# Optimization experiments

Hardware: AMD Instinct MI355X
Metric: run time of the kernel (lower is better)

## Reference

```python
import jax, jax.numpy as jnp
import numpy as np

B, N, C = 2, 2048, 768
H = 12
HD = C // H
SCALE = HD ** -0.5


def setup_inputs() -> dict:
    key = jax.random.key(0)
    ks = jax.random.split(key, 5)
    s = 1.0 / np.sqrt(C)
    return {
        "x": jax.random.normal(ks[0], (B, N, C), dtype=jnp.float32),
        "Wq": jax.random.normal(ks[1], (C, C), dtype=jnp.float32) * s,
        "Wk": jax.random.normal(ks[2], (C, C), dtype=jnp.float32) * s,
        "Wv": jax.random.normal(ks[3], (C, C), dtype=jnp.float32) * s,
        "Wo": jax.random.normal(ks[4], (C, C), dtype=jnp.float32) * s,
        "bo": jnp.zeros((C,), dtype=jnp.float32),
    }


def reference(x, Wq, Wk, Wv, Wo, bo):
    b, n, c = x.shape
    # projections (equinox Linear: y = W @ x, i.e. x @ W.T); split heads -> [b, h, n, hd]
    q = (x @ Wq.T).reshape(b, n, H, HD).transpose(0, 2, 1, 3)
    k = (x @ Wk.T).reshape(b, n, H, HD).transpose(0, 2, 1, 3)
    v = (x @ Wv.T).reshape(b, n, H, HD).transpose(0, 2, 1, 3)
    # full O(N^2) score matrix, scaled dot-product
    scores = jnp.einsum("bhqd,bhkd->bhqk", q, k) * SCALE  # [b, h, n, n]
    probs = jax.nn.softmax(scores, axis=-1)
    # attn_drop = 0.0 -> identity
    out = jnp.einsum("bhqk,bhkd->bhqd", probs, v)  # [b, h, n, hd]
    out = out.transpose(0, 2, 1, 3).reshape(b, n, c)
    # output projection (proj_drop = 0.0 -> identity)
    return out @ Wo.T + bo
```

## Files before the change

kernel.cpp:

```cpp
#include <hip/hip_runtime.h>
#include <hip/hip_bf16.h>
#include <cstdint>

typedef __bf16 bf16;
typedef bf16 bf16x8 __attribute__((ext_vector_type(8)));
typedef float f32x4 __attribute__((ext_vector_type(4)));
typedef uint32_t u32;

#define MFMA16(a, b, c) __builtin_amdgcn_mfma_f32_16x16x32_bf16(a, b, c, 0, 0, 0)

static constexpr int Bb = 2, Hh = 12, Nn = 2048, Cc = 768, HD = 64;
static constexpr float SCALE_L2E = 0.125f * 1.4426950408889634f;

__device__ inline u32 pkbf(float a, float b) {
    union { struct { uint16_t lo, hi; } s; u32 w; } u;
    u.s.lo = __builtin_bit_cast(uint16_t, (bf16)a);
    u.s.hi = __builtin_bit_cast(uint16_t, (bf16)b);
    return u.w;
}

__device__ __forceinline__ size_t fidx(int bh, int n, int hd) {
    return ((size_t)(bh * 128 + (n >> 4)) * 2 + (hd >> 5)) * 512 +
           (size_t)(((hd >> 3) & 3) * 128 + (n & 15) * 8 + (hd & 7));
}
__device__ __forceinline__ size_t vidx(int bh, int n, int hd) {
    return (((size_t)(bh * 32 + (n >> 6)) * 4 + (hd >> 4)) * 2 + ((n >> 5) & 1)) * 512 +
           (size_t)(((n >> 3) & 3) * 128 + (hd & 15) * 8 + (n & 7));
}

__device__ __forceinline__ void stage16(const bf16* g, bf16* l) {
    __builtin_amdgcn_global_load_lds(
        (const __attribute__((address_space(1))) void*)g,
        (__attribute__((address_space(3))) void*)l, 16, 0, 0);
}

__device__ __forceinline__ void gload(bf16x8& d, const bf16* p) {
    asm volatile("global_load_dwordx4 %0, %1, off" : "=v"(d) : "v"(p));
}

#define VMWAIT(N) do { asm volatile("s_waitcnt vmcnt(" #N ")" ::); \
                       __builtin_amdgcn_sched_barrier(0); } while (0)

__global__ __launch_bounds__(256) void cvt_all(const float* __restrict__ x,
                                               const float* __restrict__ wq,
                                               const float* __restrict__ wk,
                                               const float* __restrict__ wv,
                                               const float* __restrict__ wo,
                                               bf16* __restrict__ xb,
                                               bf16* __restrict__ wqkv,
                                               bf16* __restrict__ wob) {
    const int b = blockIdx.x;
    const float* src;
    bf16* dst;
    int i;
    if (b < 1536) {
        src = x; dst = xb; i = b * 256 + threadIdx.x;
    } else {
        const int wbid  = b - 1536;
        const int which = wbid / 288;
        src = which == 0 ? wq : which == 1 ? wk : which == 2 ? wv : wo;
        dst = which == 3 ? wob : wqkv + (size_t)which * 589824;
        i = (wbid % 288) * 256 + threadIdx.x;
    }
    const float4* p = reinterpret_cast<const float4*>(src) + (size_t)i * 2;
    float4 v0 = p[0], v1 = p[1];
    bf16x8 o;
    o[0] = (bf16)v0.x; o[1] = (bf16)v0.y; o[2] = (bf16)v0.z; o[3] = (bf16)v0.w;
    o[4] = (bf16)v1.x; o[5] = (bf16)v1.y; o[6] = (bf16)v1.z; o[7] = (bf16)v1.w;
    reinterpret_cast<bf16x8*>(dst)[i] = o;
}

__global__ __launch_bounds__(256, 3) void gemm_qkv(const bf16* __restrict__ X,
                                                   const bf16* __restrict__ W,
                                                   bf16* __restrict__ QF,
                                                   bf16* __restrict__ KF,
                                                   bf16* __restrict__ VF) {
    const int m0      = blockIdx.x * 128;
    const int j00     = blockIdx.y * 128;
    const int grp     = blockIdx.y / 6;
    const int colbase = (blockIdx.y % 6) * 128;
    const int w   = threadIdx.x >> 6;
    const int wr  = w >> 1;
    const int wc  = w & 1;
    const int l   = threadIdx.x & 63;
    const int lr  = l & 15;
    const int lg  = l >> 4;

    __shared__ bf16 lsA[2][128 * 32];
    __shared__ bf16 lsB[2][128 * 32];

    const int lrow = l >> 2;
    const int lcol = (l & 3) * 8;

    auto STAGE = [&](int buf, int kk) {
#pragma unroll
        for (int i = 0; i < 2; i++) {
            const int s = w * 2 + i;
            stage16(X + (size_t)(m0 + s * 16 + lrow) * Cc + kk + lcol, &lsA[buf][s * 512]);
            stage16(W + (size_t)(j00 + s * 16 + lrow) * Cc + kk + lcol, &lsB[buf][s * 512]);
        }
    };

    f32x4 acc[4][4] = {};

    STAGE(0, 0);
    __syncthreads();
    int cur = 0;
#pragma unroll 1
    for (int it = 0; it < 24; ++it) {
        if (it < 23) STAGE(cur ^ 1, (it + 1) * 32);
        bf16x8 a[4], b[4];
#pragma unroll
        for (int r = 0; r < 4; r++)
            a[r] = *reinterpret_cast<const bf16x8*>(&lsA[cur][(wr * 64 + r * 16 + lr) * 32 + lg * 8]);
#pragma unroll
        for (int c = 0; c < 4; c++)
            b[c] = *reinterpret_cast<const bf16x8*>(&lsB[cur][(wc * 64 + c * 16 + lr) * 32 + lg * 8]);
        __builtin_amdgcn_s_setprio(1);
#pragma unroll
        for (int r = 0; r < 4; r++)
#pragma unroll
            for (int c = 0; c < 4; c++)
                acc[r][c] = MFMA16(a[r], b[c], acc[r][c]);
        __builtin_amdgcn_s_setprio(0);
        __syncthreads();
        cur ^= 1;
    }

#pragma unroll
    for (int r = 0; r < 4; r++)
#pragma unroll
        for (int c = 0; c < 4; c++)
#pragma unroll
            for (int j = 0; j < 4; j++) {
                const int m   = m0 + wr * 64 + r * 16 + lg * 4 + j;
                const int col = colbase + wc * 64 + c * 16 + lr;
                const int bb = m >> 11, n = m & 2047;
                const int h = col >> 6, hd = col & 63;
                const int bh = bb * Hh + h;
                const float v = acc[r][c][j];
                if (grp == 0) {
                    QF[fidx(bh, n, hd)] = (bf16)(v * SCALE_L2E);
                } else if (grp == 1) {
                    KF[fidx(bh, n, hd)] = (bf16)v;
                } else {
                    VF[vidx(bh, n, hd)] = (bf16)v;
                }
            }
}

__global__ __launch_bounds__(256) void gemm_proj(const bf16* __restrict__ X,
                                                 const bf16* __restrict__ W,
                                                 const float* __restrict__ bias,
                                                 float* __restrict__ Y) {
    const int m0 = blockIdx.x * 64;
    const int j0 = blockIdx.y * 64;
    const int w  = threadIdx.x >> 6;
    const int l  = threadIdx.x & 63;
    const int lr = l & 15;
    const int lg = l >> 4;

    __shared__ bf16 lsA[2][64 * 32];
    __shared__ bf16 lsB[2][64 * 32];

    const int lrow = l >> 2;
    const int lcol = (l & 3) * 8;

    auto STAGE = [&](int buf, int kk) {
        stage16(X + (size_t)(m0 + w * 16 + lrow) * Cc + kk + lcol, &lsA[buf][w * 512]);
        stage16(W + (size_t)(j0 + w * 16 + lrow) * Cc + kk + lcol, &lsB[buf][w * 512]);
    };

    f32x4 acc[4] = {};

    STAGE(0, 0);
    __syncthreads();
    int cur = 0;
#pragma unroll 1
    for (int it = 0; it < 24; ++it) {
        if (it < 23) STAGE(cur ^ 1, (it + 1) * 32);
        bf16x8 a = *reinterpret_cast<const bf16x8*>(&lsA[cur][(w * 16 + lr) * 32 + lg * 8]);
        bf16x8 b[4];
#pragma unroll
        for (int c = 0; c < 4; c++)
            b[c] = *reinterpret_cast<const bf16x8*>(&lsB[cur][(c * 16 + lr) * 32 + lg * 8]);
        __builtin_amdgcn_s_setprio(1);
#pragma unroll
        for (int c = 0; c < 4; c++)
            acc[c] = MFMA16(a, b[c], acc[c]);
        __builtin_amdgcn_s_setprio(0);
        __syncthreads();
        cur ^= 1;
    }

    const int mw = m0 + w * 16;
#pragma unroll
    for (int c = 0; c < 4; c++)
#pragma unroll
        for (int j = 0; j < 4; j++) {
            const int m   = mw + lg * 4 + j;
            const int col = j0 + c * 16 + lr;
            Y[(size_t)m * Cc + col] = acc[c][j] + bias[col];
        }
}

__global__ __launch_bounds__(256, 3) void attn_kernel(const bf16* __restrict__ QF,
                                                      const bf16* __restrict__ KF,
                                                      const bf16* __restrict__ VF,
                                                      bf16* __restrict__ AO) {
    const int bid  = (blockIdx.x & 7) * 96 + (blockIdx.x >> 3);
    const int qb   = bid & 31;
    const int bh   = bid >> 5;
    const int tid  = threadIdx.x;
    const int wid  = tid >> 6;
    const int team = wid >> 1;
    const int wt   = wid & 1;
    const int l    = tid & 63;
    const int lr   = l & 15;
    const int lg   = l >> 4;

    __shared__ bf16 vbuf[2][2][4096];
    __shared__ u32  p_lds[4][2][576];

    f32x4 acc[2][4] = {};
    f32x4 accs[2] = {};

    const bf16* Qbase = QF + ((size_t)(bh * 128 + qb * 4 + wt * 2) * 2) * 512 + l * 8;
    const bf16x8 qa0 = *reinterpret_cast<const bf16x8*>(Qbase);
    const bf16x8 qb0 = *reinterpret_cast<const bf16x8*>(Qbase + 512);
    const bf16x8 qa1 = *reinterpret_cast<const bf16x8*>(Qbase + 1024);
    const bf16x8 qb1 = *reinterpret_cast<const bf16x8*>(Qbase + 1536);

    bf16x8 ONES;
#pragma unroll
    for (int i = 0; i < 8; i++) ONES[i] = (bf16)1.0f;

    bf16x8 ka[8];
    const int tbase = team * 16;

    auto loadK = [&](int t) {
        const bf16* p = KF + ((size_t)bh * 256 + (tbase + t) * 8) * 512 + l * 8;
#pragma unroll
        for (int s = 0; s < 8; s++)
            gload(ka[s], p + (size_t)s * 512);
    };
    auto stageV = [&](int slot, int t) {
        const size_t tb = ((size_t)bh * 256 + (tbase + t) * 8) * 512;
#pragma unroll
        for (int i = 0; i < 4; i++) {
            const int s = wt * 4 + i;
            stage16(VF + tb + (size_t)s * 512 + l * 8, &vbuf[team][slot][s * 512]);
        }
    };

    const f32x4 fz = {0.f, 0.f, 0.f, 0.f};

    auto EXPPACK = [&](int f, const f32x4* s) {
#pragma unroll
        for (int st = 0; st < 4; st++) {
            float p0 = exp2f(s[st][0]);
            float p1 = exp2f(s[st][1]);
            float p2 = exp2f(s[st][2]);
            float p3 = exp2f(s[st][3]);
            *reinterpret_cast<uint2*>(&p_lds[wid][f][lr * 36 + st * 8 + lg * 2]) =
                make_uint2(pkbf(p0, p1), pkbf(p2, p3));
        }
    };

    stageV(0, 0);
    loadK(0);

#pragma unroll 1
    for (int t = 0; t < 16; ++t) {
        VMWAIT(0);
        __builtin_amdgcn_s_barrier();

        f32x4 s[4];
        __builtin_amdgcn_s_setprio(1);
#pragma unroll
        for (int st = 0; st < 4; st++) {
            s[st] = MFMA16(ka[st * 2], qa0, fz);
            s[st] = MFMA16(ka[st * 2 + 1], qb0, s[st]);
        }
        __builtin_amdgcn_s_setprio(0);
        EXPPACK(0, s);
        __builtin_amdgcn_s_setprio(1);
#pragma unroll
        for (int st = 0; st < 4; st++) {
            s[st] = MFMA16(ka[st * 2], qa1, fz);
            s[st] = MFMA16(ka[st * 2 + 1], qb1, s[st]);
        }
        __builtin_amdgcn_s_setprio(0);
        if (t < 15) {
            loadK(t + 1);
            stageV((t + 1) & 1, t + 1);
        }
        EXPPACK(1, s);

        asm volatile("s_waitcnt lgkmcnt(0)" ::: "memory");
        __builtin_amdgcn_sched_barrier(0);
        const bf16x8 pa00 = *reinterpret_cast<const bf16x8*>(&p_lds[wid][0][lr * 36 + lg * 4]);
        const bf16x8 pa01 = *reinterpret_cast<const bf16x8*>(&p_lds[wid][0][lr * 36 + 16 + lg * 4]);
        const bf16x8 pa10 = *reinterpret_cast<const bf16x8*>(&p_lds[wid][1][lr * 36 + lg * 4]);
        const bf16x8 pa11 = *reinterpret_cast<const bf16x8*>(&p_lds[wid][1][lr * 36 + 16 + lg * 4]);

        const bf16* vb = &vbuf[team][t & 1][l * 8];
        __builtin_amdgcn_s_setprio(1);
#pragma unroll
        for (int c = 0; c < 4; c++) {
            bf16x8 v0 = *reinterpret_cast<const bf16x8*>(vb + (c * 2) * 512);
            bf16x8 v1 = *reinterpret_cast<const bf16x8*>(vb + (c * 2 + 1) * 512);
            acc[0][c] = MFMA16(v0, pa00, acc[0][c]);
            acc[0][c] = MFMA16(v1, pa01, acc[0][c]);
            acc[1][c] = MFMA16(v0, pa10, acc[1][c]);
            acc[1][c] = MFMA16(v1, pa11, acc[1][c]);
        }
        accs[0] = MFMA16(ONES, pa00, accs[0]);
        accs[0] = MFMA16(ONES, pa01, accs[0]);
        accs[1] = MFMA16(ONES, pa10, accs[1]);
        accs[1] = MFMA16(ONES, pa11, accs[1]);
        __builtin_amdgcn_s_setprio(0);
    }

    __syncthreads();
    float* mrg = reinterpret_cast<float*>(&p_lds[0][0][0]);
    if (team == 1) {
#pragma unroll
        for (int f = 0; f < 2; f++) {
            float* slot = mrg + (wt * 2 + f) * 1088 + l * 17;
#pragma unroll
            for (int c = 0; c < 4; c++)
#pragma unroll
                for (int j = 0; j < 4; j++) slot[c * 4 + j] = acc[f][c][j];
            slot[16] = accs[f][0];
        }
    }
    __syncthreads();
    if (team == 1) return;

    const int bb = bh / Hh, h = bh % Hh;
#pragma unroll
    for (int f = 0; f < 2; f++) {
        const float* slot = mrg + (wt * 2 + f) * 1088 + l * 17;
#pragma unroll
        for (int c = 0; c < 4; c++)
#pragma unroll
            for (int j = 0; j < 4; j++) acc[f][c][j] += slot[c * 4 + j];
        const float rtot = accs[f][0] + slot[16];
        const float rinv = 1.0f / rtot;

        float* o_lds = reinterpret_cast<float*>(&vbuf[0][0][0]) + (wt * 2 + f) * 1088;
#pragma unroll
        for (int c = 0; c < 4; c++)
#pragma unroll
            for (int j = 0; j < 4; j++)
                o_lds[(c * 16 + lg * 4 + j) * 17 + lr] = acc[f][c][j] * rinv;
        asm volatile("s_waitcnt lgkmcnt(0)" ::: "memory");
        __builtin_amdgcn_sched_barrier(0);

        const int q0 = qb * 64 + (wt * 2 + f) * 16;
        const int qq = l >> 2, dc = (l & 3) * 16;
        bf16x8 o0, o1;
#pragma unroll
        for (int dd = 0; dd < 8; dd++) o0[dd] = (bf16)o_lds[(dc + dd) * 17 + qq];
#pragma unroll
        for (int dd = 0; dd < 8; dd++) o1[dd] = (bf16)o_lds[(dc + 8 + dd) * 17 + qq];
        bf16* dst = AO + ((size_t)(bb * Nn) + q0 + qq) * Cc + h * 64 + dc;
        *reinterpret_cast<bf16x8*>(dst) = o0;
        *reinterpret_cast<bf16x8*>(dst + 8) = o1;
    }
}

extern "C" void kernel_launch(void* const* d_in, const int* in_sizes, int n_in,
                              void* d_out, int out_size, void* d_ws, size_t ws_size,
                              hipStream_t stream) {
    const float* x  = (const float*)d_in[0];
    const float* Wq = (const float*)d_in[1];
    const float* Wk = (const float*)d_in[2];
    const float* Wv = (const float*)d_in[3];
    const float* Wo = (const float*)d_in[4];
    const float* bo = (const float*)d_in[5];

    const size_t XB    = 0;
    const size_t WQKVB = XB + 6291456;
    const size_t WOB   = WQKVB + 3538944;
    const size_t QB    = WOB + 1179648;
    const size_t KB    = QB + 6291456;
    const size_t VTB   = KB + 6291456;
    const size_t AOB   = VTB + 6291456;
    const size_t NEED  = AOB + 6291456;
    if (ws_size < NEED) return;

    char* ws = (char*)d_ws;
    bf16* xb   = (bf16*)(ws + XB);
    bf16* wqkv = (bf16*)(ws + WQKVB);
    bf16* wob  = (bf16*)(ws + WOB);
    bf16* QF   = (bf16*)(ws + QB);
    bf16* KF   = (bf16*)(ws + KB);
    bf16* VF   = (bf16*)(ws + VTB);
    bf16* AOb  = (bf16*)(ws + AOB);

    cvt_all<<<2688, 256, 0, stream>>>(x, Wq, Wk, Wv, Wo, xb, wqkv, wob);

    gemm_qkv<<<dim3(32, 18), 256, 0, stream>>>(xb, wqkv, QF, KF, VF);

    attn_kernel<<<768, 256, 0, stream>>>(QF, KF, VF, AOb);

    gemm_proj<<<dim3(64, 12), 256, 0, stream>>>(AOb, wob, bo, (float*)d_out);
}
```

Measured before the change: 97.02 us.

## Load V tiles straight into registers and drop LDS staging and barrier

V fragments are now loaded per wave directly into registers with global loads, replacing the double-buffered LDS staging that was shared across a wave pair. This removes the per-iteration block barrier and the LDS round trip for V. The loads are software-pipelined with vmcnt waits, K for the next tile issued mid-iteration and V for the next tile at the end. In exchange each wave fetches the full V tile, so global V traffic doubles. Register use also rises, so launch bounds drop from 3 to 2 blocks per CU, and the output transpose buffer is moved into the merge LDS region.

```diff
diff --git a/kernel.cpp b/kernel.cpp
--- a/kernel.cpp
+++ b/kernel.cpp
@@ -204,7 +204,7 @@
         }
 }
 
-__global__ __launch_bounds__(256, 3) void attn_kernel(const bf16* __restrict__ QF,
+__global__ __launch_bounds__(256, 2) void attn_kernel(const bf16* __restrict__ QF,
                                                       const bf16* __restrict__ KF,
                                                       const bf16* __restrict__ VF,
                                                       bf16* __restrict__ AO) {
@@ -219,8 +219,7 @@
     const int lr   = l & 15;
     const int lg   = l >> 4;
 
-    __shared__ bf16 vbuf[2][2][4096];
-    __shared__ u32  p_lds[4][2][576];
+    __shared__ u32 p_lds[4][2][576];
 
     f32x4 acc[2][4] = {};
     f32x4 accs[2] = {};
@@ -235,7 +234,7 @@
 #pragma unroll
     for (int i = 0; i < 8; i++) ONES[i] = (bf16)1.0f;
 
-    bf16x8 ka[8];
+    bf16x8 ka[8], vv[8];
     const int tbase = team * 16;
 
     auto loadK = [&](int t) {
@@ -244,13 +243,11 @@
         for (int s = 0; s < 8; s++)
             gload(ka[s], p + (size_t)s * 512);
     };
-    auto stageV = [&](int slot, int t) {
-        const size_t tb = ((size_t)bh * 256 + (tbase + t) * 8) * 512;
-#pragma unroll
-        for (int i = 0; i < 4; i++) {
-            const int s = wt * 4 + i;
-            stage16(VF + tb + (size_t)s * 512 + l * 8, &vbuf[team][slot][s * 512]);
-        }
+    auto loadV = [&](int t) {
+        const bf16* p = VF + ((size_t)bh * 256 + (tbase + t) * 8) * 512 + l * 8;
+#pragma unroll
+        for (int s = 0; s < 8; s++)
+            gload(vv[s], p + (size_t)s * 512);
     };
 
     const f32x4 fz = {0.f, 0.f, 0.f, 0.f};
@@ -267,13 +264,12 @@
         }
     };
 
-    stageV(0, 0);
     loadK(0);
+    loadV(0);
 
 #pragma unroll 1
     for (int t = 0; t < 16; ++t) {
-        VMWAIT(0);
-        __builtin_amdgcn_s_barrier();
+        VMWAIT(8);
 
         f32x4 s[4];
         __builtin_amdgcn_s_setprio(1);
@@ -291,10 +287,7 @@
             s[st] = MFMA16(ka[st * 2 + 1], qb1, s[st]);
         }
         __builtin_amdgcn_s_setprio(0);
-        if (t < 15) {
-            loadK(t + 1);
-            stageV((t + 1) & 1, t + 1);
-        }
+        if (t < 15) loadK(t + 1);
         EXPPACK(1, s);
 
         asm volatile("s_waitcnt lgkmcnt(0)" ::: "memory");
@@ -304,22 +297,21 @@
         const bf16x8 pa10 = *reinterpret_cast<const bf16x8*>(&p_lds[wid][1][lr * 36 + lg * 4]);
         const bf16x8 pa11 = *reinterpret_cast<const bf16x8*>(&p_lds[wid][1][lr * 36 + 16 + lg * 4]);
 
-        const bf16* vb = &vbuf[team][t & 1][l * 8];
+        VMWAIT(8);
         __builtin_amdgcn_s_setprio(1);
 #pragma unroll
         for (int c = 0; c < 4; c++) {
-            bf16x8 v0 = *reinterpret_cast<const bf16x8*>(vb + (c * 2) * 512);
-            bf16x8 v1 = *reinterpret_cast<const bf16x8*>(vb + (c * 2 + 1) * 512);
-            acc[0][c] = MFMA16(v0, pa00, acc[0][c]);
-            acc[0][c] = MFMA16(v1, pa01, acc[0][c]);
-            acc[1][c] = MFMA16(v0, pa10, acc[1][c]);
-            acc[1][c] = MFMA16(v1, pa11, acc[1][c]);
+            acc[0][c] = MFMA16(vv[c * 2], pa00, acc[0][c]);
+            acc[0][c] = MFMA16(vv[c * 2 + 1], pa01, acc[0][c]);
+            acc[1][c] = MFMA16(vv[c * 2], pa10, acc[1][c]);
+            acc[1][c] = MFMA16(vv[c * 2 + 1], pa11, acc[1][c]);
         }
         accs[0] = MFMA16(ONES, pa00, accs[0]);
         accs[0] = MFMA16(ONES, pa01, accs[0]);
         accs[1] = MFMA16(ONES, pa10, accs[1]);
         accs[1] = MFMA16(ONES, pa11, accs[1]);
         __builtin_amdgcn_s_setprio(0);
+        if (t < 15) loadV(t + 1);
     }
 
     __syncthreads();
@@ -348,8 +340,10 @@
             for (int j = 0; j < 4; j++) acc[f][c][j] += slot[c * 4 + j];
         const float rtot = accs[f][0] + slot[16];
         const float rinv = 1.0f / rtot;
-
-        float* o_lds = reinterpret_cast<float*>(&vbuf[0][0][0]) + (wt * 2 + f) * 1088;
+        asm volatile("s_waitcnt lgkmcnt(0)" ::: "memory");
+        __builtin_amdgcn_sched_barrier(0);
+
+        float* o_lds = mrg + (wt * 2 + f) * 1088;
 #pragma unroll
         for (int c = 0; c < 4; c++)
 #pragma unroll
```

Result: faster. 94.69 us (-2.4%).
